# Kernel tuning notes

Measured on AMD Instinct MI355X. Metric: run time of the kernel, lower is better.

Reference implementation:

```python
import jax, jax.numpy as jnp
import numpy as np
import math

B, L, WIN, D, H, FF, NL, V, M = 16, 2048, 128, 512, 8, 2048, 3, 32000, 32
HD = D // H
EPS = 1e-5
RECON_W = 0.1

def _ln(x, g, b):
    m = x.mean(-1, keepdims=True)
    v = ((x - m) ** 2).mean(-1, keepdims=True)
    return (x - m) * jax.lax.rsqrt(v + EPS) * g + b

def _denoiser(x_t, t, motif, left, right, glob, time_proj_W, time_proj_b, cond_proj_W, cond_proj_b,
              qkv_W, qkv_b, attn_out_W, attn_out_b, ff1_W, ff1_b, ff2_W, ff2_b,
              ln1_g, ln1_b, ln2_g, ln2_b, out_W, out_b):
    half = D // 2
    freqs = jnp.exp(-math.log(10000.0) * jnp.arange(half) / (half - 1))
    a = t[:, None] * freqs[None, :]
    temb = jnp.concatenate([jnp.sin(a), jnp.cos(a)], -1) @ time_proj_W.T + time_proj_b
    x = x_t + temb[:, None, :]
    cond = jnp.concatenate([motif, left, right, glob], -1) @ cond_proj_W.T + cond_proj_b
    x = jnp.concatenate([cond[:, None, :], x], 1)
    S = x.shape[1]
    for i in range(NL):  # post-norm TransformerEncoderLayer, relu, no dropout (eval)
        qkv = x @ qkv_W[i].T + qkv_b[i]
        q, k, v = jnp.split(qkv, 3, axis=-1)
        q = q.reshape(B, S, H, HD); k = k.reshape(B, S, H, HD); v = v.reshape(B, S, H, HD)
        attn = jax.nn.softmax(jnp.einsum('bqhd,bkhd->bhqk', q, k) / math.sqrt(HD), axis=-1)
        ctx = jnp.einsum('bhqk,bkhd->bqhd', attn, v).reshape(B, S, D)
        x = _ln(x + ctx @ attn_out_W[i].T + attn_out_b[i], ln1_g[i], ln1_b[i])
        h = jax.nn.relu(x @ ff1_W[i].T + ff1_b[i]) @ ff2_W[i].T + ff2_b[i]
        x = _ln(x + h, ln2_g[i], ln2_b[i])
    return x[:, 1:, :] @ out_W.T + out_b

def setup_inputs():
    key = jax.random.key(0)
    ks = jax.random.split(key, 20)
    s = 0.02
    inp = {}
    inp['token_ids'] = jax.random.randint(ks[0], (B, L), 0, V)
    inp['motif_ids'] = jax.random.randint(ks[1], (B, M), 0, V)
    inp['motif_len'] = jax.random.randint(ks[2], (B,), 1, M + 1)
    inp['window_start'] = jax.random.randint(ks[3], (B,), 0, L - WIN)
    lens = jax.random.randint(ks[4], (B,), 1, WIN + 1).at[0].set(WIN)
    inp['window_end'] = inp['window_start'] + lens
    inp['t'] = jax.random.uniform(ks[5], (B,))
    inp['x0'] = jax.random.normal(ks[6], (B, WIN, D))
    inp['embed_table'] = jax.random.normal(ks[7], (V, D)) * s
    inp['decode_W'] = jax.random.normal(ks[8], (V, D)) * s
    inp['decode_b'] = jnp.zeros((V,))
    inp['adapter_W'] = jax.random.normal(ks[9], (D, D)) * s
    inp['adapter_b'] = jnp.zeros((D,))
    inp['time_proj_W'] = jax.random.normal(ks[10], (D, D)) * s
    inp['time_proj_b'] = jnp.zeros((D,))
    inp['cond_proj_W'] = jax.random.normal(ks[11], (D, 4 * D)) * s
    inp['cond_proj_b'] = jnp.zeros((D,))
    inp['qkv_W'] = jax.random.normal(ks[12], (NL, 3 * D, D)) * s
    inp['qkv_b'] = jnp.zeros((NL, 3 * D))
    inp['attn_out_W'] = jax.random.normal(ks[13], (NL, D, D)) * s
    inp['attn_out_b'] = jnp.zeros((NL, D))
    inp['ff1_W'] = jax.random.normal(ks[14], (NL, FF, D)) * s
    inp['ff1_b'] = jnp.zeros((NL, FF))
    inp['ff2_W'] = jax.random.normal(ks[15], (NL, D, FF)) * s
    inp['ff2_b'] = jnp.zeros((NL, D))
    inp['ln1_g'] = jnp.ones((NL, D)); inp['ln1_b'] = jnp.zeros((NL, D))
    inp['ln2_g'] = jnp.ones((NL, D)); inp['ln2_b'] = jnp.zeros((NL, D))
    inp['out_W'] = jax.random.normal(ks[16], (D, D)) * s
    inp['out_b'] = jnp.zeros((D,))
    return inp

def _forward(token_ids, motif_ids, motif_len, window_start, window_end, t, x0,
             embed_table, decode_W, decode_b, adapter_W, adapter_b, den):
    hidden = embed_table[token_ids]  # frozen backbone encode: [B, L, D]
    pos = jnp.arange(L)
    def pool(s, e):  # vectorized masked mean over region [s, e)
        m = ((pos[None, :] >= s[:, None]) & (pos[None, :] < e[:, None])).astype(hidden.dtype)
        return jnp.einsum('bl,bld->bd', m, hidden) / jnp.maximum(m.sum(1, keepdims=True), 1.0)
    left = pool(jnp.zeros_like(window_start), window_start)
    right = pool(window_end, jnp.full_like(window_end, L))
    glob = hidden.mean(1)
    memb = embed_table[motif_ids]
    mmask = (jnp.arange(M)[None, :] < motif_len[:, None]).astype(memb.dtype)
    motif = (memb * mmask[..., None]).sum(1) / jnp.maximum(motif_len.astype(memb.dtype), 1.0)[:, None]
    actual = jnp.clip(window_end - window_start, 0, WIN)
    win_mask = jnp.arange(WIN)[None, :] < actual[:, None]
    idx = jnp.clip(window_start[:, None] + jnp.arange(WIN)[None, :], 0, L - 1)
    x1 = jnp.take_along_axis(hidden, idx[:, :, None], axis=1) * win_mask[..., None]
    x_t = (1 - t[:, None, None]) * x0 + t[:, None, None] * x1
    target_v = x1 - x0
    pred_v = _denoiser(x_t, t, motif, left, right, glob, *den)
    valid = win_mask[..., None].astype(x1.dtype)
    vel = (((pred_v - target_v) ** 2) * valid).sum() / (jnp.maximum(valid.sum(), 1.0) * D)
    pred_x1 = x_t + (1 - t[:, None, None]) * pred_v
    logits = (pred_x1 @ adapter_W.T + adapter_b) @ decode_W.T + decode_b
    labels = jnp.where(win_mask, jnp.take_along_axis(token_ids, idx, axis=1), -100)
    lv = labels != -100
    logp = jax.nn.log_softmax(logits, axis=-1)
    picked = jnp.take_along_axis(logp, jnp.maximum(labels, 0)[..., None], axis=-1)[..., 0]
    recon = -(picked * lv).sum() / jnp.maximum(lv.sum(), 1)
    return vel + RECON_W * recon

def reference(token_ids, motif_ids, motif_len, window_start, window_end, t, x0,
              embed_table, decode_W, decode_b, adapter_W, adapter_b,
              time_proj_W, time_proj_b, cond_proj_W, cond_proj_b, qkv_W, qkv_b,
              attn_out_W, attn_out_b, ff1_W, ff1_b, ff2_W, ff2_b,
              ln1_g, ln1_b, ln2_g, ln2_b, out_W, out_b):
    den = (time_proj_W, time_proj_b, cond_proj_W, cond_proj_b, qkv_W, qkv_b,
           attn_out_W, attn_out_b, ff1_W, ff1_b, ff2_W, ff2_b,
           ln1_g, ln1_b, ln2_g, ln2_b, out_W, out_b)
    return _forward(token_ids, motif_ids, motif_len, window_start, window_end, t, x0,
                    embed_table, decode_W, decode_b, adapter_W, adapter_b, den)
```

## Files before the change

kernel.cpp:

```cpp
#include <hip/hip_runtime.h>
#include <hip/hip_bf16.h>
#include <math.h>

typedef __hip_bfloat16 bf16;

constexpr int cB = 16, cL = 2048, cWIN = 128, cD = 512, cH = 8, cFF = 2048;
constexpr int cNL = 3, cV = 32000, cM = 32;
constexpr int cHD = cD / cH;
constexpr int cS = cWIN + 1;
constexpr float cEPS = 1e-5f;
constexpr float cRECON_W = 0.1f;
constexpr int cNVT = cV / 128;

__device__ __forceinline__ float b2f(bf16 x) { return __bfloat162float(x); }

__device__ __forceinline__ float ldx(const void* p, size_t i, int f32) {
    return f32 ? ((const float*)p)[i]
               : __bfloat162float(((const bf16*)p)[i]);
}

__device__ __forceinline__ unsigned int f2bf(float f) {
    union { float f; unsigned int u; } v; v.f = f;
    unsigned int u = v.u + 0x7FFFu + ((v.u >> 16) & 1u);
    return u >> 16;
}

__device__ __forceinline__ void glds16(const unsigned short* g, unsigned short* l) {
    __builtin_amdgcn_global_load_lds(
        (const __attribute__((address_space(1))) void*)g,
        (__attribute__((address_space(3))) void*)l, 16, 0, 0);
}

typedef short bf16x8 __attribute__((ext_vector_type(8)));
typedef float f32x4  __attribute__((ext_vector_type(4)));

__global__ void detect_kernel(const void* __restrict__ x0raw, int* __restrict__ flag)
{
    const unsigned short* h = (const unsigned short*)x0raw;
    int tid = threadIdx.x;
    int cnt = 0;
    for (int j = tid; j < 8192; j += 256) {
        unsigned short u = h[2 * j];
        int e = (u >> 7) & 0xFF;
        if (e >= 134) cnt++;
    }
    __shared__ int red[256];
    red[tid] = cnt; __syncthreads();
    for (int off = 128; off > 0; off >>= 1) {
        if (tid < off) red[tid] += red[tid + off];
        __syncthreads();
    }
    if (tid == 0) *flag = (red[0] > 400) ? 1 : 0;
}

__global__ __launch_bounds__(512) void pools_part_kernel(
    const int* __restrict__ tok, const int* __restrict__ wstart,
    const int* __restrict__ wend, const void* __restrict__ emb,
    float* __restrict__ part, const int* __restrict__ dflag)
{
    const int f32 = *dflag;
    int chunk = blockIdx.x;
    int b = blockIdx.y;
    int d = threadIdx.x;
    int ws_ = wstart[b], we_ = wend[b];
    float sl = 0.f, sr = 0.f, sg = 0.f;
    int l0 = chunk * 128;
    for (int l = l0; l < l0 + 128; ++l) {
        int t = tok[b * cL + l];
        float h = ldx(emb, (size_t)t * cD + d, f32);
        sg += h;
        if (l < ws_) sl += h;
        if (l >= we_) sr += h;
    }
    size_t base = ((size_t)(b * 16 + chunk)) * 3 * cD;
    part[base + d]            = sl;
    part[base + cD + d]       = sr;
    part[base + 2 * cD + d]   = sg;
}

__global__ __launch_bounds__(512) void pools_combine_kernel(
    const float* __restrict__ part, const int* __restrict__ mids,
    const int* __restrict__ mlen, const int* __restrict__ wstart,
    const int* __restrict__ wend, const void* __restrict__ emb,
    unsigned short* __restrict__ featb, const void* __restrict__ t_arr,
    unsigned short* __restrict__ tfbb, const int* __restrict__ tok,
    int* __restrict__ labels, const int* __restrict__ dflag)
{
    const int f32 = *dflag;
    int b = blockIdx.x;
    int d = threadIdx.x;
    int ws_ = wstart[b], we_ = wend[b];
    float sl = 0.f, sr = 0.f, sg = 0.f;
    for (int c = 0; c < 16; ++c) {
        size_t base = ((size_t)(b * 16 + c)) * 3 * cD;
        sl += part[base + d];
        sr += part[base + cD + d];
        sg += part[base + 2 * cD + d];
    }
    int ml = mlen[b];
    float sm = 0.f;
    for (int j = 0; j < cM; ++j) {
        if (j < ml) sm += ldx(emb, (size_t)mids[b * cM + j] * cD + d, f32);
    }
    unsigned short* fr = featb + (size_t)b * (4 * cD);
    fr[d]            = (unsigned short)f2bf(sm / fmaxf((float)ml, 1.f));
    fr[cD + d]       = (unsigned short)f2bf(sl / fmaxf((float)ws_, 1.f));
    fr[2 * cD + d]   = (unsigned short)f2bf(sr / fmaxf((float)(cL - we_), 1.f));
    fr[3 * cD + d]   = (unsigned short)f2bf(sg / (float)cL);

    {
        float t = ldx(t_arr, b, f32);
        const int half = cD / 2;
        float v;
        if (d < half) {
            float frq = expf(-logf(10000.f) * (float)d / (float)(half - 1));
            v = sinf(t * frq);
        } else {
            float frq = expf(-logf(10000.f) * (float)(d - half) / (float)(half - 1));
            v = cosf(t * frq);
        }
        tfbb[(size_t)b * cD + d] = (unsigned short)f2bf(v);
    }

    if (d < cWIN) {
        int actual = min(max(we_ - ws_, 0), cWIN);
        labels[b * cWIN + d] =
            (d < actual) ? tok[b * cL + min(ws_ + d, cL - 1)] : -1;
    }
}

__global__ __launch_bounds__(512) void build_x_kernel(
    const int* __restrict__ tok, const int* __restrict__ wstart,
    const int* __restrict__ wend, const void* __restrict__ t_arr,
    const void* __restrict__ x0, const void* __restrict__ emb,
    const float* __restrict__ cond, const float* __restrict__ temb,
    float* __restrict__ x, unsigned short* __restrict__ xbf,
    float* __restrict__ x1, float* __restrict__ xt,
    const int* __restrict__ dflag)
{
    const int f32 = *dflag;
    int row = blockIdx.x;
    int b = row / cS, s = row % cS;
    int d = threadIdx.x;
    if (s == 0) {
        float cv = cond[b * cD + d];
        x[(size_t)row * cD + d] = cv;
        xbf[(size_t)row * cD + d] = (unsigned short)f2bf(cv);
        return;
    }
    int i = s - 1;
    int ws_ = wstart[b], we_ = wend[b];
    int actual = min(max(we_ - ws_, 0), cWIN);
    int idx = min(ws_ + i, cL - 1);
    float x1v = 0.f;
    if (i < actual) x1v = ldx(emb, (size_t)tok[b * cL + idx] * cD + d, f32);
    float t = ldx(t_arr, b, f32);
    float x0v = ldx(x0, ((size_t)b * cWIN + i) * cD + d, f32);
    float xtv = (1.f - t) * x0v + t * x1v;
    size_t ro = ((size_t)b * cWIN + i) * cD + d;
    x1[ro] = x1v;
    xt[ro] = xtv;
    float xv = xtv + temb[b * cD + d];
    x[(size_t)row * cD + d] = xv;
    xbf[(size_t)row * cD + d] = (unsigned short)f2bf(xv);
}

constexpr int GL2 = 72;
__global__ __launch_bounds__(512) void gemm_bf(
    const unsigned short* __restrict__ Abf, const void* __restrict__ Wb,
    size_t wOff, const void* __restrict__ biasb, size_t bOff,
    float* __restrict__ Cf, unsigned short* __restrict__ Cbf,
    int Mdim, int Ndim, int Kdim, int relu, int obf, int amap,
    const int* __restrict__ dflag)
{
    const int f32 = *dflag;
    const float* Wf = (const float*)Wb + wOff;
    const unsigned short* Wh = (const unsigned short*)Wb + wOff;
    __shared__ unsigned short As[2][64 * GL2];
    __shared__ unsigned short Bs[2][64 * GL2];
    const int tid = threadIdx.x;
    const int lane = tid & 63;
    const int wid = tid >> 6;
    const int wm = wid >> 1;
    const int wn = wid & 1;
    const int quad = lane >> 4, lm = lane & 15;
    const int m0 = blockIdx.y * 64;
    const int n0 = blockIdx.x * 64;

    f32x4 acc0 = (f32x4){0.f, 0.f, 0.f, 0.f};
    f32x4 acc1 = (f32x4){0.f, 0.f, 0.f, 0.f};

    const int srow = tid >> 3;
    const int sc8  = (tid & 7) * 8;
    const int ssw  = ((tid & 7) ^ ((tid >> 3) & 7)) * 8;
    const int lmm  = lm & 7;

    auto loadA = [&](int k0, uint4& r) {
        int r0 = m0 + srow;
        uint4 v = {0u, 0u, 0u, 0u};
        if (r0 < Mdim) {
            size_t ar = amap ? ((size_t)(r0 >> 7) * cS + 1 + (r0 & 127))
                             : (size_t)r0;
            v = *(const uint4*)(Abf + ar * Kdim + k0 + sc8);
        }
        r = v;
    };
    auto loadB = [&](int k0, uint4& r) {
        size_t g = (size_t)(n0 + srow) * Kdim + k0 + sc8;
        if (f32) {
            float4 v0 = *(const float4*)(Wf + g);
            float4 v1 = *(const float4*)(Wf + g + 4);
            r = make_uint4(
                f2bf(v0.x) | (f2bf(v0.y) << 16), f2bf(v0.z) | (f2bf(v0.w) << 16),
                f2bf(v1.x) | (f2bf(v1.y) << 16), f2bf(v1.z) | (f2bf(v1.w) << 16));
        } else {
            r = *(const uint4*)(Wh + g);
        }
    };
    auto stores = [&](int buf, const uint4& ra, const uint4& rb) {
        *(uint4*)(&As[buf][srow * GL2 + ssw]) = ra;
        *(uint4*)(&Bs[buf][srow * GL2 + ssw]) = rb;
    };
    auto compute = [&](int buf) {
        #pragma unroll
        for (int kk = 0; kk < 2; ++kk) {
            const int sl = ((kk * 4 + quad) ^ lmm) * 8;
            bf16x8 a0 = *(const bf16x8*)(&As[buf][(wm * 16 + lm) * GL2 + sl]);
            bf16x8 b0 = *(const bf16x8*)(&Bs[buf][(wn * 32 + lm) * GL2 + sl]);
            bf16x8 b1 = *(const bf16x8*)(&Bs[buf][(wn * 32 + 16 + lm) * GL2 + sl]);
            acc0 = __builtin_amdgcn_mfma_f32_16x16x32_bf16(a0, b0, acc0, 0, 0, 0);
            acc1 = __builtin_amdgcn_mfma_f32_16x16x32_bf16(a0, b1, acc1, 0, 0, 0);
        }
    };

    uint4 raA, rbA, raB, rbB;
    loadA(0, raA);  loadB(0, rbA);
    loadA(64, raB); loadB(64, rbB);
    const int nk = Kdim >> 6;
    for (int t = 0; t < nk; t += 2) {
        stores(0, raA, rbA);
        __syncthreads();
        if (t + 2 < nk) { loadA((t + 2) * 64, raA); loadB((t + 2) * 64, rbA); }
        compute(0);
        stores(1, raB, rbB);
        __syncthreads();
        if (t + 3 < nk) { loadA((t + 3) * 64, raB); loadB((t + 3) * 64, rbB); }
        compute(1);
    }

    #pragma unroll
    for (int in = 0; in < 2; ++in) {
        int gc = n0 + wn * 32 + in * 16 + lm;
        float bv = ldx(biasb, bOff + gc, f32);
        const f32x4& a = in ? acc1 : acc0;
        #pragma unroll
        for (int r = 0; r < 4; ++r) {
            int gr = m0 + wm * 16 + quad * 4 + r;
            if (gr < Mdim) {
                float v = a[r] + bv;
                if (relu) v = fmaxf(v, 0.f);
                if (obf) Cbf[(size_t)gr * Ndim + gc] = (unsigned short)f2bf(v);
                else     Cf[(size_t)gr * Ndim + gc] = v;
            }
        }
    }
}

__global__ __launch_bounds__(256) void attn_mfma_kernel(
    const unsigned short* __restrict__ qkv, unsigned short* __restrict__ ctx)
{
    constexpr int SP = 160;
    constexpr int KP = 72;
    constexpr int VP = 168;
    const int h = blockIdx.x, b = blockIdx.y, z = blockIdx.z;
    const int tid = threadIdx.x;
    const int lane = tid & 63;
    const int wid = tid >> 6;
    const int quad = lane >> 4, lm = lane & 15;

    __shared__ unsigned short Ks[SP * KP];
    __shared__ unsigned short Vt[64 * VP];
    __shared__ unsigned short Pl[4 * 16 * VP];

    const unsigned short* base = qkv + (size_t)b * cS * (3 * cD) + h * cHD;

    for (int c = tid; c < SP * 8; c += 256) {
        int row = c >> 3, g = c & 7;
        uint4 v = {0u, 0u, 0u, 0u};
        if (row < cS)
            v = *(const uint4*)(base + (size_t)row * (3 * cD) + cD + g * 8);
        *(uint4*)(Ks + row * KP + g * 8) = v;
    }
    for (int c = tid; c < SP * 16; c += 256) {
        int key = c >> 4, d4 = c & 15;
        uint2 v = {0u, 0u};
        if (key < cS)
            v = *(const uint2*)(base + (size_t)key * (3 * cD) + 2 * cD + d4 * 4);
        Vt[(d4 * 4 + 0) * VP + key] = (unsigned short)(v.x & 0xFFFFu);
        Vt[(d4 * 4 + 1) * VP + key] = (unsigned short)(v.x >> 16);
        Vt[(d4 * 4 + 2) * VP + key] = (unsigned short)(v.y & 0xFFFFu);
        Vt[(d4 * 4 + 3) * VP + key] = (unsigned short)(v.y >> 16);
    }
    __syncthreads();

    unsigned short* Pw = Pl + wid * (16 * VP);
    const int t = z * 3 + wid;

    if (wid < 3 && t < 9) {
        int qs = t * 16 + lm;
        bf16x8 aq[2];
        #pragma unroll
        for (int j = 0; j < 8; ++j) { aq[0][j] = 0; aq[1][j] = 0; }
        if (qs < cS) {
            const unsigned short* qrow = base + (size_t)qs * (3 * cD);
            aq[0] = *(const bf16x8*)(qrow + quad * 8);
            aq[1] = *(const bf16x8*)(qrow + 32 + quad * 8);
        }

        f32x4 sc[10];
        #pragma unroll
        for (int n = 0; n < 10; ++n) {
            sc[n] = (f32x4){0.f, 0.f, 0.f, 0.f};
            bf16x8 bk0 = *(const bf16x8*)(Ks + (n * 16 + lm) * KP + quad * 8);
            sc[n] = __builtin_amdgcn_mfma_f32_16x16x32_bf16(aq[0], bk0, sc[n], 0, 0, 0);
            bf16x8 bk1 = *(const bf16x8*)(Ks + (n * 16 + lm) * KP + 32 + quad * 8);
            sc[n] = __builtin_amdgcn_mfma_f32_16x16x32_bf16(aq[1], bk1, sc[n], 0, 0, 0);
        }

        #pragma unroll
        for (int r = 0; r < 4; ++r) {
            float mx = -3.0e38f;
            #pragma unroll
            for (int n = 0; n < 10; ++n) {
                float v = sc[n][r] * 0.125f;
                mx = fmaxf(mx, ((n * 16 + lm) < cS) ? v : -3.0e38f);
            }
            #pragma unroll
            for (int msk = 1; msk < 16; msk <<= 1)
                mx = fmaxf(mx, __shfl_xor(mx, msk));
            float p[10];
            float sum = 0.f;
            #pragma unroll
            for (int n = 0; n < 10; ++n) {
                float e = ((n * 16 + lm) < cS) ? expf(sc[n][r] * 0.125f - mx) : 0.f;
                p[n] = e; sum += e;
            }
            #pragma unroll
            for (int msk = 1; msk < 16; msk <<= 1)
                sum += __shfl_xor(sum, msk);
            float inv = 1.f / sum;
            unsigned short* pr = Pw + (quad * 4 + r) * VP + lm;
            #pragma unroll
            for (int n = 0; n < 10; ++n)
                pr[n * 16] = (unsigned short)f2bf(p[n] * inv);
        }

        asm volatile("s_waitcnt lgkmcnt(0)" ::: "memory");
        __builtin_amdgcn_sched_barrier(0);

        f32x4 o[4];
        #pragma unroll
        for (int j = 0; j < 4; ++j) o[j] = (f32x4){0.f, 0.f, 0.f, 0.f};
        #pragma unroll
        for (int ks = 0; ks < 5; ++ks) {
            bf16x8 ap = *(const bf16x8*)(Pw + lm * VP + ks * 32 + quad * 8);
            #pragma unroll
            for (int j = 0; j < 4; ++j) {
                bf16x8 bv = *(const bf16x8*)(Vt + (j * 16 + lm) * VP + ks * 32 + quad * 8);
                o[j] = __builtin_amdgcn_mfma_f32_16x16x32_bf16(ap, bv, o[j], 0, 0, 0);
            }
        }

        #pragma unroll
        for (int r = 0; r < 4; ++r) {
            int s_ = t * 16 + quad * 4 + r;
            if (s_ < cS) {
                unsigned short* orow = ctx + ((size_t)(b * cS + s_)) * cD + h * cHD;
                #pragma unroll
                for (int j = 0; j < 4; ++j)
                    orow[j * 16 + lm] = (unsigned short)f2bf(o[j][r]);
            }
        }
    }
}

__global__ __launch_bounds__(256) void resid_ln_kernel(
    float* __restrict__ x, const float* __restrict__ h,
    const void* __restrict__ g, const void* __restrict__ bta, size_t off,
    unsigned short* __restrict__ xbf, const int* __restrict__ dflag)
{
    const int f32 = *dflag;
    int row = blockIdx.x;
    int tid = threadIdx.x;
    __shared__ float red[256];
    float v[2];
    float s = 0.f;
    #pragma unroll
    for (int j = 0; j < 2; ++j) {
        int d = tid + j * 256;
        v[j] = x[(size_t)row * cD + d] + h[(size_t)row * cD + d];
        s += v[j];
    }
    red[tid] = s; __syncthreads();
    for (int o = 128; o > 0; o >>= 1) {
        if (tid < o) red[tid] += red[tid + o];
        __syncthreads();
    }
    float mean = red[0] / (float)cD;
    __syncthreads();
    float vs = 0.f;
    #pragma unroll
    for (int j = 0; j < 2; ++j) { float dd = v[j] - mean; vs += dd * dd; }
    red[tid] = vs; __syncthreads();
    for (int o = 128; o > 0; o >>= 1) {
        if (tid < o) red[tid] += red[tid + o];
        __syncthreads();
    }
    float rs = rsqrtf(red[0] / (float)cD + cEPS);
    #pragma unroll
    for (int j = 0; j < 2; ++j) {
        int d = tid + j * 256;
        float ov = (v[j] - mean) * rs * ldx(g, off + d, f32) + ldx(bta, off + d, f32);
        x[(size_t)row * cD + d] = ov;
        xbf[(size_t)row * cD + d] = (unsigned short)f2bf(ov);
    }
}

__global__ __launch_bounds__(512) void predvel_kernel(
    const float* __restrict__ xt, const float* __restrict__ pv,
    const float* __restrict__ x1, const void* __restrict__ x0,
    const void* __restrict__ t_arr, const int* __restrict__ wstart,
    const int* __restrict__ wend, unsigned short* __restrict__ px1,
    float* __restrict__ velpart, const int* __restrict__ dflag)
{
    const int f32 = *dflag;
    int row = blockIdx.x;
    int b = row >> 7, i = row & 127;
    int d = threadIdx.x;
    float t = ldx(t_arr, b, f32);
    size_t o = (size_t)row * cD + d;
    float pvv = pv[o];
    px1[o] = (unsigned short)f2bf(xt[o] + (1.f - t) * pvv);
    int actual = min(max(wend[b] - wstart[b], 0), cWIN);
    float s = 0.f;
    if (i < actual) {
        float tv = x1[o] - ldx(x0, o, f32);
        float diff = pvv - tv;
        s = diff * diff;
    }
    __shared__ float red[512];
    red[d] = s; __syncthreads();
    for (int off = 256; off > 0; off >>= 1) {
        if (d < off) red[d] += red[d + off];
        __syncthreads();
    }
    if (d == 0) velpart[row] = red[0];
}

__global__ __launch_bounds__(256) void cvt_w_kernel(
    const void* __restrict__ Wsrc, unsigned short* __restrict__ dst,
    const int* __restrict__ dflag)
{
    if (!*dflag) return;
    const float4* src = (const float4*)Wsrc;
    size_t n4 = (size_t)cV * cD / 4;
    for (size_t i = (size_t)blockIdx.x * 256 + threadIdx.x; i < n4;
         i += (size_t)gridDim.x * 256) {
        float4 v = src[i];
        unsigned int p0 = f2bf(v.x) | (f2bf(v.y) << 16);
        unsigned int p1 = f2bf(v.z) | (f2bf(v.w) << 16);
        ((uint2*)dst)[i] = make_uint2(p0, p1);
    }
}

__global__ __launch_bounds__(256) void decode_mfma2_kernel(
    const unsigned short* __restrict__ hbf, const unsigned short* __restrict__ wbf,
    const void* __restrict__ dW, const void* __restrict__ db,
    const int* __restrict__ labels,
    float* __restrict__ pm, float* __restrict__ ps, float* __restrict__ lab,
    const int* __restrict__ dflag)
{
    const int f32 = *dflag;
    const unsigned short* Wsrc = f32 ? wbf : (const unsigned short*)dW;
    const int bid = blockIdx.x;
    const int xcd = bid & 7;
    const int local = bid >> 3;
    const int nt = xcd * 32 + (local >> 4);
    const int mt = local & 15;
    if (nt >= cNVT) return;
    const int m0 = mt * 128, n0 = nt * 128;

    __shared__ __align__(16) char smem[17408];
    unsigned short* As = (unsigned short*)smem;
    unsigned short* Bs = As + 4096;

    const int tid = threadIdx.x;
    const int lane = tid & 63;
    const int wid = tid >> 6;
    const int wm = wid >> 1, wn = wid & 1;
    const int quad = lane >> 4, lm = lane & 15;

    const int grow  = lane >> 2;
    const int gslot = (lane & 3) ^ ((lane >> 3) & 3);
    const int rslot = (quad ^ ((lm >> 1) & 3)) * 8;

    const unsigned short* gA = hbf  + (size_t)(m0 + wid * 32 + grow) * cD + gslot * 8;
    const unsigned short* gB = Wsrc + (size_t)(n0 + wid * 32 + grow) * cD + gslot * 8;

    f32x4 acc[4][4];
    #pragma unroll
    for (int i = 0; i < 4; ++i)
        #pragma unroll
        for (int j = 0; j < 4; ++j)
            acc[i][j] = (f32x4){0.f, 0.f, 0.f, 0.f};

    for (int k0 = 0; k0 < cD; k0 += 32) {
        #pragma unroll
        for (int c = 0; c < 2; ++c) {
            glds16(gA + (size_t)c * 16 * cD + k0, As + (wid * 2 + c) * 512);
            glds16(gB + (size_t)c * 16 * cD + k0, Bs + (wid * 2 + c) * 512);
        }
        __syncthreads();
        bf16x8 af[4], bfr[4];
        #pragma unroll
        for (int im = 0; im < 4; ++im)
            af[im] = *(const bf16x8*)(As + (wm * 64 + im * 16 + lm) * 32 + rslot);
        #pragma unroll
        for (int in = 0; in < 4; ++in)
            bfr[in] = *(const bf16x8*)(Bs + (wn * 64 + in * 16 + lm) * 32 + rslot);
        #pragma unroll
        for (int im = 0; im < 4; ++im)
            #pragma unroll
            for (int in = 0; in < 4; ++in)
                acc[im][in] = __builtin_amdgcn_mfma_f32_16x16x32_bf16(
                    af[im], bfr[in], acc[im][in], 0, 0, 0);
        __syncthreads();
    }

    float bv[4];
    #pragma unroll
    for (int in = 0; in < 4; ++in)
        bv[in] = ldx(db, n0 + wn * 64 + in * 16 + lm, f32);
    #pragma unroll
    for (int im = 0; im < 4; ++im)
        #pragma unroll
        for (int in = 0; in < 4; ++in)
            #pragma unroll
            for (int r = 0; r < 4; ++r)
                acc[im][in][r] += bv[in];

    #pragma unroll
    for (int im = 0; im < 4; ++im) {
        #pragma unroll
        for (int r = 0; r < 4; ++r) {
            int gr = m0 + wm * 64 + im * 16 + quad * 4 + r;
            int lb = labels[gr];
            #pragma unroll
            for (int in = 0; in < 4; ++in) {
                int col = n0 + wn * 64 + in * 16 + lm;
                if (lb == col) lab[gr] = acc[im][in][r];
            }
        }
    }

    float (*red)[33] = (float(*)[33])smem;
    float* mrow = (float*)(smem + 16896);
    #pragma unroll
    for (int im = 0; im < 4; ++im) {
        #pragma unroll
        for (int r = 0; r < 4; ++r) {
            int rl = wm * 64 + im * 16 + quad * 4 + r;
            float mx = acc[im][0][r];
            #pragma unroll
            for (int in = 1; in < 4; ++in) mx = fmaxf(mx, acc[im][in][r]);
            red[rl][wn * 16 + lm] = mx;
        }
    }
    __syncthreads();
    if (tid < 128) {
        float mx = red[tid][0];
        #pragma unroll
        for (int t = 1; t < 32; ++t) mx = fmaxf(mx, red[tid][t]);
        mrow[tid] = mx;
    }
    __syncthreads();
    #pragma unroll
    for (int im = 0; im < 4; ++im) {
        #pragma unroll
        for (int r = 0; r < 4; ++r) {
            int rl = wm * 64 + im * 16 + quad * 4 + r;
            float m_ = mrow[rl];
            float s = 0.f;
            #pragma unroll
            for (int in = 0; in < 4; ++in) s += expf(acc[im][in][r] - m_);
            red[rl][wn * 16 + lm] = s;
        }
    }
    __syncthreads();
    if (tid < 128) {
        float s = red[tid][0];
        #pragma unroll
        for (int t = 1; t < 32; ++t) s += red[tid][t];
        int gr = m0 + tid;
        pm[(size_t)gr * cNVT + nt] = mrow[tid];
        ps[(size_t)gr * cNVT + nt] = s;
    }
}

constexpr int GLDS = 40;
__global__ __launch_bounds__(256) void decode_mfma_kernel(
    const unsigned short* __restrict__ hbf, const void* __restrict__ dW,
    const void* __restrict__ db, const int* __restrict__ labels,
    float* __restrict__ pm, float* __restrict__ ps, float* __restrict__ lab,
    const int* __restrict__ dflag)
{
    const int f32 = *dflag;
    const float* Wf = (const float*)dW;
    const unsigned short* Wh = (const unsigned short*)dW;
    __shared__ unsigned short As[128 * GLDS];
    __shared__ unsigned short Bs[128 * GLDS];
    const int tid = threadIdx.x;
    const int lane = tid & 63;
    const int wid = tid >> 6;
    const int wm = wid >> 1, wn = wid & 1;
    const int quad = lane >> 4, lm = lane & 15;
    const int nt = blockIdx.x;
    const int mt = blockIdx.y;
    const int m0 = mt * 128, n0 = nt * 128;

    f32x4 acc[4][4];
    #pragma unroll
    for (int i = 0; i < 4; ++i)
        #pragma unroll
        for (int j = 0; j < 4; ++j)
            acc[i][j] = (f32x4){0.f, 0.f, 0.f, 0.f};

    for (int k0 = 0; k0 < cD; k0 += 32) {
        #pragma unroll
        for (int t = 0; t < 2; ++t) {
            int idx = tid + t * 256;
            int row = idx >> 2, c = idx & 3;
            uint4 v = *(const uint4*)(hbf + (size_t)(m0 + row) * cD + k0 + c * 8);
            *(uint4*)(As + row * GLDS + c * 8) = v;
        }
        #pragma unroll
        for (int t = 0; t < 4; ++t) {
            int chunk = tid + t * 256;
            int row = chunk >> 3;
            int kc = (chunk & 7) * 4;
            size_t gro = (size_t)(n0 + row) * cD + k0 + kc;
            if (f32) {
                float4 v = *(const float4*)(Wf + gro);
                unsigned int p0 = f2bf(v.x) | (f2bf(v.y) << 16);
                unsigned int p1 = f2bf(v.z) | (f2bf(v.w) << 16);
                *(uint2*)(Bs + row * GLDS + kc) = make_uint2(p0, p1);
            } else {
                *(uint2*)(Bs + row * GLDS + kc) = *(const uint2*)(Wh + gro);
            }
        }
        __syncthreads();
        bf16x8 af[4], bfr[4];
        #pragma unroll
        for (int im = 0; im < 4; ++im) {
            int row = wm * 64 + im * 16 + lm;
            af[im] = *(const bf16x8*)(As + row * GLDS + quad * 8);
        }
        #pragma unroll
        for (int in = 0; in < 4; ++in) {
            int row = wn * 64 + in * 16 + lm;
            bfr[in] = *(const bf16x8*)(Bs + row * GLDS + quad * 8);
        }
        #pragma unroll
        for (int im = 0; im < 4; ++im)
            #pragma unroll
            for (int in = 0; in < 4; ++in)
                acc[im][in] = __builtin_amdgcn_mfma_f32_16x16x32_bf16(
                    af[im], bfr[in], acc[im][in], 0, 0, 0);
        __syncthreads();
    }

    float bv[4];
    #pragma unroll
    for (int in = 0; in < 4; ++in)
        bv[in] = ldx(db, n0 + wn * 64 + in * 16 + lm, f32);
    #pragma unroll
    for (int im = 0; im < 4; ++im)
        #pragma unroll
        for (int in = 0; in < 4; ++in)
            #pragma unroll
            for (int r = 0; r < 4; ++r)
                acc[im][in][r] += bv[in];

    #pragma unroll
    for (int im = 0; im < 4; ++im) {
        #pragma unroll
        for (int r = 0; r < 4; ++r) {
            int gr = m0 + wm * 64 + im * 16 + quad * 4 + r;
            int lb = labels[gr];
            #pragma unroll
            for (int in = 0; in < 4; ++in) {
                int col = n0 + wn * 64 + in * 16 + lm;
                if (lb == col) lab[gr] = acc[im][in][r];
            }
        }
    }

    __shared__ float red[128][33];
    __shared__ float mrow[128];
    #pragma unroll
    for (int im = 0; im < 4; ++im) {
        #pragma unroll
        for (int r = 0; r < 4; ++r) {
            int rl = wm * 64 + im * 16 + quad * 4 + r;
            float mx = acc[im][0][r];
            #pragma unroll
            for (int in = 1; in < 4; ++in) mx = fmaxf(mx, acc[im][in][r]);
            red[rl][wn * 16 + lm] = mx;
        }
    }
    __syncthreads();
    if (tid < 128) {
        float mx = red[tid][0];
        #pragma unroll
        for (int t = 1; t < 32; ++t) mx = fmaxf(mx, red[tid][t]);
        mrow[tid] = mx;
    }
    __syncthreads();
    #pragma unroll
    for (int im = 0; im < 4; ++im) {
        #pragma unroll
        for (int r = 0; r < 4; ++r) {
            int rl = wm * 64 + im * 16 + quad * 4 + r;
            float m_ = mrow[rl];
            float s = 0.f;
            #pragma unroll
            for (int in = 0; in < 4; ++in) s += expf(acc[im][in][r] - m_);
            red[rl][wn * 16 + lm] = s;
        }
    }
    __syncthreads();
    if (tid < 128) {
        float s = red[tid][0];
        #pragma unroll
        for (int t = 1; t < 32; ++t) s += red[tid][t];
        int gr = m0 + tid;
        pm[(size_t)gr * cNVT + nt] = mrow[tid];
        ps[(size_t)gr * cNVT + nt] = s;
    }
}

__global__ __launch_bounds__(64) void lse_reduce_kernel(
    const float* __restrict__ pm, const float* __restrict__ ps,
    const float* __restrict__ lab, const int* __restrict__ labels,
    float* __restrict__ logppart)
{
    int r = blockIdx.x;
    int tid = threadIdx.x;
    if (labels[r] < 0) {
        if (tid == 0) logppart[r] = 0.f;
        return;
    }
    float m = -1e30f;
    for (int c = tid; c < cNVT; c += 64) m = fmaxf(m, pm[(size_t)r * cNVT + c]);
    for (int off = 32; off > 0; off >>= 1) m = fmaxf(m, __shfl_down(m, off));
    m = __shfl(m, 0);
    float s = 0.f;
    for (int c = tid; c < cNVT; c += 64)
        s += ps[(size_t)r * cNVT + c] * expf(pm[(size_t)r * cNVT + c] - m);
    for (int off = 32; off > 0; off >>= 1) s += __shfl_down(s, off);
    if (tid == 0) logppart[r] = lab[r] - (m + logf(s));
}

__global__ __launch_bounds__(256) void finalize_kernel(
    const float* __restrict__ velpart, const float* __restrict__ logppart,
    const int* __restrict__ wstart, const int* __restrict__ wend,
    void* __restrict__ out, const int* __restrict__ dflag)
{
    const int f32 = *dflag;
    __shared__ float r1[256], r2[256];
    int tid = threadIdx.x;
    float s1 = 0.f, s2 = 0.f;
    for (int r = tid; r < cB * cWIN; r += 256) {
        s1 += velpart[r];
        s2 += logppart[r];
    }
    r1[tid] = s1; r2[tid] = s2; __syncthreads();
    for (int off = 128; off > 0; off >>= 1) {
        if (tid < off) { r1[tid] += r1[tid + off]; r2[tid] += r2[tid + off]; }
        __syncthreads();
    }
    if (tid == 0) {
        float cnt = 0.f;
        for (int b = 0; b < cB; ++b)
            cnt += (float)min(max(wend[b] - wstart[b], 0), cWIN);
        cnt = fmaxf(cnt, 1.f);
        float vel = r1[0] / (cnt * (float)cD);
        float recon = -r2[0] / cnt;
        float loss = vel + cRECON_W * recon;
        if (f32) ((float*)out)[0] = loss;
        else     ((bf16*)out)[0] = __float2bfloat16(loss);
    }
}

extern "C" void kernel_launch(void* const* d_in, const int* in_sizes, int n_in,
                              void* d_out, int out_size, void* d_ws, size_t ws_size,
                              hipStream_t stream) {
    const int*  token_ids    = (const int*)d_in[0];
    const int*  motif_ids    = (const int*)d_in[1];
    const int*  motif_len    = (const int*)d_in[2];
    const int*  window_start = (const int*)d_in[3];
    const int*  window_end   = (const int*)d_in[4];
    const void* t_arr        = d_in[5];
    const void* x0           = d_in[6];
    const void* embed_table  = d_in[7];
    const void* decode_W     = d_in[8];
    const void* decode_b     = d_in[9];
    const void* adapter_W    = d_in[10];
    const void* adapter_b    = d_in[11];
    const void* time_proj_W  = d_in[12];
    const void* time_proj_b  = d_in[13];
    const void* cond_proj_W  = d_in[14];
    const void* cond_proj_b  = d_in[15];
    const void* qkv_W        = d_in[16];
    const void* qkv_b        = d_in[17];
    const void* attn_out_W   = d_in[18];
    const void* attn_out_b   = d_in[19];
    const void* ff1_W        = d_in[20];
    const void* ff1_b        = d_in[21];
    const void* ff2_W        = d_in[22];
    const void* ff2_b        = d_in[23];
    const void* ln1_g        = d_in[24];
    const void* ln1_b        = d_in[25];
    const void* ln2_g        = d_in[26];
    const void* ln2_b        = d_in[27];
    const void* out_W        = d_in[28];
    const void* out_b        = d_in[29];

    float* w = (float*)d_ws;
    const size_t SZ_X   = (size_t)cB * cS * cD;
    const size_t SZ_BA  = (size_t)cB * cS * cFF;
    const size_t SZ_ROW = (size_t)cB * cWIN * cD;
    float* x     = w;
    float* bufA  = x + SZ_X;
    float* bufB  = bufA + SZ_BA;
    float* bufC  = bufB + SZ_X;
    float* x1b   = bufC + SZ_X;
    float* xtb   = x1b + SZ_ROW;
    float* pvb   = xtb + SZ_ROW;
    float* h2b   = pvb + SZ_ROW;
    float* feat  = h2b + SZ_ROW;
    float* tfb   = feat + (size_t)cB * 4 * cD;
    float* cond  = tfb + (size_t)cB * cD;
    float* temb  = cond + (size_t)cB * cD;
    float* velpart = temb + (size_t)cB * cD;
    float* logppart = velpart + (size_t)cB * cWIN;
    int*   dflag = (int*)(logppart + (size_t)cB * cWIN);
    int*   labels = (int*)(dflag + 16);
    float* wsend = (float*)(labels + (size_t)cB * cWIN);
    unsigned short* wbf = (unsigned short*)wsend;

    const size_t need_bytes = ((char*)wsend - (char*)d_ws)
                            + (size_t)cV * cD * sizeof(unsigned short) + 256;
    const bool fast_decode = ws_size >= need_bytes;

    const int Wrows = cB * cWIN;
    const int Mrows = cB * cS;

    unsigned short* xbf    = (unsigned short*)h2b;
    unsigned short* featbf = xbf + (size_t)Mrows * cD;
    unsigned short* tfbbf  = featbf + (size_t)cB * 4 * cD;
    unsigned short* qkvbf  = (unsigned short*)bufA;
    unsigned short* ff1bf  = (unsigned short*)bufA;
    unsigned short* ctxbf  = (unsigned short*)bufB;
    unsigned short* px1bf  = (unsigned short*)(bufA + (size_t)3 * 1024 * 1024);
    unsigned short* hbf    = (unsigned short*)bufC;

    float* pm  = bufA;
    float* ps  = pm + (size_t)Wrows * cNVT;
    float* lab = ps + (size_t)Wrows * cNVT;
    float* poolspart = bufC;

    auto gemm = [&](const unsigned short* A, const void* W, size_t wOff,
                    const void* bias, size_t bOff, float* Cf, unsigned short* Cbf,
                    int M_, int N_, int K_, int relu, int obf, int amap) {
        dim3 grid(N_ / 64, (M_ + 63) / 64);
        gemm_bf<<<grid, 512, 0, stream>>>(A, W, wOff, bias, bOff, Cf, Cbf,
                                          M_, N_, K_, relu, obf, amap, dflag);
    };

    detect_kernel<<<1, 256, 0, stream>>>(x0, dflag);
    if (fast_decode)
        cvt_w_kernel<<<2048, 256, 0, stream>>>(decode_W, wbf, dflag);
    pools_part_kernel<<<dim3(16, cB), cD, 0, stream>>>(token_ids, window_start,
        window_end, embed_table, poolspart, dflag);
    pools_combine_kernel<<<cB, cD, 0, stream>>>(poolspart, motif_ids, motif_len,
        window_start, window_end, embed_table, featbf, t_arr, tfbbf,
        token_ids, labels, dflag);
    gemm(featbf, cond_proj_W, 0, cond_proj_b, 0, cond, nullptr, cB, cD, 4 * cD, 0, 0, 0);
    gemm(tfbbf, time_proj_W, 0, time_proj_b, 0, temb, nullptr, cB, cD, cD, 0, 0, 0);
    build_x_kernel<<<Mrows, cD, 0, stream>>>(token_ids, window_start, window_end,
        t_arr, x0, embed_table, cond, temb, x, xbf, x1b, xtb, dflag);

    for (int i = 0; i < cNL; ++i) {
        gemm(xbf, qkv_W, (size_t)i * 3 * cD * cD, qkv_b, (size_t)i * 3 * cD,
             nullptr, qkvbf, Mrows, 3 * cD, cD, 0, 1, 0);
        attn_mfma_kernel<<<dim3(cH, cB, 3), 256, 0, stream>>>(qkvbf, ctxbf);
        gemm(ctxbf, attn_out_W, (size_t)i * cD * cD, attn_out_b, (size_t)i * cD,
             bufC, nullptr, Mrows, cD, cD, 0, 0, 0);
        resid_ln_kernel<<<Mrows, 256, 0, stream>>>(x, bufC, ln1_g, ln1_b,
             (size_t)i * cD, xbf, dflag);
        gemm(xbf, ff1_W, (size_t)i * cFF * cD, ff1_b, (size_t)i * cFF,
             nullptr, ff1bf, Mrows, cFF, cD, 1, 1, 0);
        gemm(ff1bf, ff2_W, (size_t)i * cD * cFF, ff2_b, (size_t)i * cD,
             bufC, nullptr, Mrows, cD, cFF, 0, 0, 0);
        resid_ln_kernel<<<Mrows, 256, 0, stream>>>(x, bufC, ln2_g, ln2_b,
             (size_t)i * cD, xbf, dflag);
    }

    gemm(xbf, out_W, 0, out_b, 0, pvb, nullptr, Wrows, cD, cD, 0, 0, 1);
    predvel_kernel<<<Wrows, 512, 0, stream>>>(xtb, pvb, x1b, x0, t_arr,
        window_start, window_end, px1bf, velpart, dflag);
    gemm(px1bf, adapter_W, 0, adapter_b, 0, nullptr, hbf, Wrows, cD, cD, 0, 1, 0);

    if (fast_decode) {
        decode_mfma2_kernel<<<4096, 256, 0, stream>>>(
            hbf, wbf, decode_W, decode_b, labels, pm, ps, lab, dflag);
    } else {
        decode_mfma_kernel<<<dim3(cNVT, Wrows / 128), 256, 0, stream>>>(
            hbf, decode_W, decode_b, labels, pm, ps, lab, dflag);
    }
    lse_reduce_kernel<<<Wrows, 64, 0, stream>>>(pm, ps, lab, labels, logppart);

    finalize_kernel<<<1, 256, 0, stream>>>(velpart, logppart,
        window_start, window_end, d_out, dflag);
}
```

Before: 803.3 us.

## Use 8 waves per decode block and shuffle-based row reductions

```diff
diff --git a/kernel.cpp b/kernel.cpp
--- a/kernel.cpp
+++ b/kernel.cpp
@@ -473,7 +473,7 @@
     }
 }
 
-__global__ __launch_bounds__(256) void decode_mfma2_kernel(
+__global__ __launch_bounds__(512) void decode_mfma2_kernel(
     const unsigned short* __restrict__ hbf, const unsigned short* __restrict__ wbf,
     const void* __restrict__ dW, const void* __restrict__ db,
     const int* __restrict__ labels,
@@ -490,61 +490,60 @@
     if (nt >= cNVT) return;
     const int m0 = mt * 128, n0 = nt * 128;
 
-    __shared__ __align__(16) char smem[17408];
-    unsigned short* As = (unsigned short*)smem;
-    unsigned short* Bs = As + 4096;
+    __shared__ __align__(16) unsigned short As[4096];
+    __shared__ __align__(16) unsigned short Bs[4096];
+    __shared__ float redw[128][4];
+    __shared__ float mrow[128];
 
     const int tid = threadIdx.x;
     const int lane = tid & 63;
     const int wid = tid >> 6;
-    const int wm = wid >> 1, wn = wid & 1;
+    const int wm = wid & 1;
+    const int wn = wid >> 1;
     const int quad = lane >> 4, lm = lane & 15;
 
     const int grow  = lane >> 2;
     const int gslot = (lane & 3) ^ ((lane >> 3) & 3);
     const int rslot = (quad ^ ((lm >> 1) & 3)) * 8;
 
-    const unsigned short* gA = hbf  + (size_t)(m0 + wid * 32 + grow) * cD + gslot * 8;
-    const unsigned short* gB = Wsrc + (size_t)(n0 + wid * 32 + grow) * cD + gslot * 8;
-
-    f32x4 acc[4][4];
+    const unsigned short* gA = hbf  + (size_t)(m0 + wid * 16 + grow) * cD + gslot * 8;
+    const unsigned short* gB = Wsrc + (size_t)(n0 + wid * 16 + grow) * cD + gslot * 8;
+
+    f32x4 acc[4][2];
     #pragma unroll
     for (int i = 0; i < 4; ++i)
         #pragma unroll
-        for (int j = 0; j < 4; ++j)
+        for (int j = 0; j < 2; ++j)
             acc[i][j] = (f32x4){0.f, 0.f, 0.f, 0.f};
 
     for (int k0 = 0; k0 < cD; k0 += 32) {
-        #pragma unroll
-        for (int c = 0; c < 2; ++c) {
-            glds16(gA + (size_t)c * 16 * cD + k0, As + (wid * 2 + c) * 512);
-            glds16(gB + (size_t)c * 16 * cD + k0, Bs + (wid * 2 + c) * 512);
-        }
-        __syncthreads();
-        bf16x8 af[4], bfr[4];
+        glds16(gA + k0, As + wid * 512);
+        glds16(gB + k0, Bs + wid * 512);
+        __syncthreads();
+        bf16x8 af[4], bfr[2];
         #pragma unroll
         for (int im = 0; im < 4; ++im)
             af[im] = *(const bf16x8*)(As + (wm * 64 + im * 16 + lm) * 32 + rslot);
         #pragma unroll
-        for (int in = 0; in < 4; ++in)
-            bfr[in] = *(const bf16x8*)(Bs + (wn * 64 + in * 16 + lm) * 32 + rslot);
+        for (int in = 0; in < 2; ++in)
+            bfr[in] = *(const bf16x8*)(Bs + (wn * 32 + in * 16 + lm) * 32 + rslot);
         #pragma unroll
         for (int im = 0; im < 4; ++im)
             #pragma unroll
-            for (int in = 0; in < 4; ++in)
+            for (int in = 0; in < 2; ++in)
                 acc[im][in] = __builtin_amdgcn_mfma_f32_16x16x32_bf16(
                     af[im], bfr[in], acc[im][in], 0, 0, 0);
         __syncthreads();
     }
 
-    float bv[4];
-    #pragma unroll
-    for (int in = 0; in < 4; ++in)
-        bv[in] = ldx(db, n0 + wn * 64 + in * 16 + lm, f32);
+    float bv[2];
+    #pragma unroll
+    for (int in = 0; in < 2; ++in)
+        bv[in] = ldx(db, n0 + wn * 32 + in * 16 + lm, f32);
     #pragma unroll
     for (int im = 0; im < 4; ++im)
         #pragma unroll
-        for (int in = 0; in < 4; ++in)
+        for (int in = 0; in < 2; ++in)
             #pragma unroll
             for (int r = 0; r < 4; ++r)
                 acc[im][in][r] += bv[in];
@@ -556,32 +555,29 @@
             int gr = m0 + wm * 64 + im * 16 + quad * 4 + r;
             int lb = labels[gr];
             #pragma unroll
-            for (int in = 0; in < 4; ++in) {
-                int col = n0 + wn * 64 + in * 16 + lm;
+            for (int in = 0; in < 2; ++in) {
+                int col = n0 + wn * 32 + in * 16 + lm;
                 if (lb == col) lab[gr] = acc[im][in][r];
             }
         }
     }
 
-    float (*red)[33] = (float(*)[33])smem;
-    float* mrow = (float*)(smem + 16896);
     #pragma unroll
     for (int im = 0; im < 4; ++im) {
         #pragma unroll
         for (int r = 0; r < 4; ++r) {
             int rl = wm * 64 + im * 16 + quad * 4 + r;
-            float mx = acc[im][0][r];
-            #pragma unroll
-            for (int in = 1; in < 4; ++in) mx = fmaxf(mx, acc[im][in][r]);
-            red[rl][wn * 16 + lm] = mx;
+            float mx = fmaxf(acc[im][0][r], acc[im][1][r]);
+            #pragma unroll
+            for (int msk = 1; msk < 16; msk <<= 1)
+                mx = fmaxf(mx, __shfl_xor(mx, msk));
+            if (lm == 0) redw[rl][wn] = mx;
         }
     }
     __syncthreads();
     if (tid < 128) {
-        float mx = red[tid][0];
-        #pragma unroll
-        for (int t = 1; t < 32; ++t) mx = fmaxf(mx, red[tid][t]);
-        mrow[tid] = mx;
+        mrow[tid] = fmaxf(fmaxf(redw[tid][0], redw[tid][1]),
+                          fmaxf(redw[tid][2], redw[tid][3]));
     }
     __syncthreads();
     #pragma unroll
@@ -590,17 +586,16 @@
         for (int r = 0; r < 4; ++r) {
             int rl = wm * 64 + im * 16 + quad * 4 + r;
             float m_ = mrow[rl];
-            float s = 0.f;
-            #pragma unroll
-            for (int in = 0; in < 4; ++in) s += expf(acc[im][in][r] - m_);
-            red[rl][wn * 16 + lm] = s;
+            float s = expf(acc[im][0][r] - m_) + expf(acc[im][1][r] - m_);
+            #pragma unroll
+            for (int msk = 1; msk < 16; msk <<= 1)
+                s += __shfl_xor(s, msk);
+            if (lm == 0) redw[rl][wn] = s;
         }
     }
     __syncthreads();
     if (tid < 128) {
-        float s = red[tid][0];
-        #pragma unroll
-        for (int t = 1; t < 32; ++t) s += red[tid][t];
+        float s = redw[tid][0] + redw[tid][1] + redw[tid][2] + redw[tid][3];
         int gr = m0 + tid;
         pm[(size_t)gr * cNVT + nt] = mrow[tid];
         ps[(size_t)gr * cNVT + nt] = s;
@@ -923,7 +918,7 @@
     gemm(px1bf, adapter_W, 0, adapter_b, 0, nullptr, hbf, Wrows, cD, cD, 0, 1, 0);
 
     if (fast_decode) {
-        decode_mfma2_kernel<<<4096, 256, 0, stream>>>(
+        decode_mfma2_kernel<<<4096, 512, 0, stream>>>(
             hbf, wbf, decode_W, decode_b, labels, pm, ps, lab, dflag);
     } else {
         decode_mfma_kernel<<<dim3(cNVT, Wrows / 128), 256, 0, stream>>>(
```

New measurement: 823.3 us. +2.5%, slower.

## Double-buffer LDS tiles in decode MFMA GEMM to overlap loads with compute

Applied to the files above, without the earlier changes.

```diff
diff --git a/kernel.cpp b/kernel.cpp
--- a/kernel.cpp
+++ b/kernel.cpp
@@ -490,9 +490,11 @@
     if (nt >= cNVT) return;
     const int m0 = mt * 128, n0 = nt * 128;
 
-    __shared__ __align__(16) char smem[17408];
-    unsigned short* As = (unsigned short*)smem;
-    unsigned short* Bs = As + 4096;
+    __shared__ __align__(16) char smem[32768];
+    unsigned short* As0 = (unsigned short*)smem;
+    unsigned short* Bs0 = As0 + 4096;
+    unsigned short* As1 = Bs0 + 4096;
+    unsigned short* Bs1 = As1 + 4096;
 
     const int tid = threadIdx.x;
     const int lane = tid & 63;
@@ -514,27 +516,42 @@
         for (int j = 0; j < 4; ++j)
             acc[i][j] = (f32x4){0.f, 0.f, 0.f, 0.f};
 
-    for (int k0 = 0; k0 < cD; k0 += 32) {
+    auto stage = [&](int k0, unsigned short* A_, unsigned short* B_) {
         #pragma unroll
         for (int c = 0; c < 2; ++c) {
-            glds16(gA + (size_t)c * 16 * cD + k0, As + (wid * 2 + c) * 512);
-            glds16(gB + (size_t)c * 16 * cD + k0, Bs + (wid * 2 + c) * 512);
-        }
-        __syncthreads();
+            glds16(gA + (size_t)c * 16 * cD + k0, A_ + (wid * 2 + c) * 512);
+            glds16(gB + (size_t)c * 16 * cD + k0, B_ + (wid * 2 + c) * 512);
+        }
+    };
+    auto compute = [&](const unsigned short* A_, const unsigned short* B_) {
         bf16x8 af[4], bfr[4];
         #pragma unroll
         for (int im = 0; im < 4; ++im)
-            af[im] = *(const bf16x8*)(As + (wm * 64 + im * 16 + lm) * 32 + rslot);
+            af[im] = *(const bf16x8*)(A_ + (wm * 64 + im * 16 + lm) * 32 + rslot);
         #pragma unroll
         for (int in = 0; in < 4; ++in)
-            bfr[in] = *(const bf16x8*)(Bs + (wn * 64 + in * 16 + lm) * 32 + rslot);
+            bfr[in] = *(const bf16x8*)(B_ + (wn * 64 + in * 16 + lm) * 32 + rslot);
         #pragma unroll
         for (int im = 0; im < 4; ++im)
             #pragma unroll
             for (int in = 0; in < 4; ++in)
                 acc[im][in] = __builtin_amdgcn_mfma_f32_16x16x32_bf16(
                     af[im], bfr[in], acc[im][in], 0, 0, 0);
-        __syncthreads();
+    };
+
+    stage(0, As0, Bs0);
+    stage(32, As1, Bs1);
+    for (int t = 0; t < 16; ++t) {
+        unsigned short* A_ = (t & 1) ? As1 : As0;
+        unsigned short* B_ = (t & 1) ? Bs1 : Bs0;
+        if (t < 15) asm volatile("s_waitcnt vmcnt(4)" ::: "memory");
+        else        asm volatile("s_waitcnt vmcnt(0)" ::: "memory");
+        __builtin_amdgcn_s_barrier();
+        compute(A_, B_);
+        asm volatile("s_waitcnt lgkmcnt(0)" ::: "memory");
+        __builtin_amdgcn_sched_barrier(0);
+        __builtin_amdgcn_s_barrier();
+        if (t + 2 < 16) stage((t + 2) * 32, A_, B_);
     }
 
     float bv[4];
```

Result: slower. 824.1 us (+2.6%).
